# Performance work log

Hardware: AMD Instinct MI355X
Metric: run time of the kernel (lower is better)

Reference implementation:

```python
import jax, jax.numpy as jnp
import numpy as np

B, H, W = 64, 512, 512
HW = H * W
MIN_, MAX_ = 100, 100          # seeds sampled per image (bg, fg)
MIN_P, MAX_P = 0.3, 0.3        # candidate-pool fractions
FG_ERODE_K, FG_ERODE_ITER = 11, 1
KSZ = 3                        # dilation kernel for seed maps
IGNORE_IDX = -255
N_BG = int(MIN_P * H * W)      # static bottom-n pool size
EPS = 1e-8


def _minpool2d(x, k):  # morphological erosion of binary map (geodesic border)
    return jax.lax.reduce_window(x, np.inf, jax.lax.min, (k, k), (1, 1), 'SAME')


def _maxpool3d(x, k):  # morphological dilation over (b,h,w)
    return jax.lax.reduce_window(x, -np.inf, jax.lax.max, (1, k, k), (1, 1, 1), 'SAME')


def _gumbel(u):
    return -jnp.log(-jnp.log(u))


def _one_sample(cam, u_fg, u_bg, th):
    # cam: [H,W] in [0,1]; u_fg/u_bg: [HW] uniform(0,1); th: scalar threshold
    cam_q = jnp.floor(cam * 255.0)
    th = jnp.where(th == 0.0, 1.0, jnp.where(th == 255.0, 254.0, th))
    deg = cam.min() == cam.max()  # degenerate map -> no seeds
    roi = (cam_q > th).astype(jnp.float32)
    for _ in range(FG_ERODE_ITER):
        roi = _minpool2d(roi, FG_ERODE_K)

    # ---- foreground: top-n of cam*roi, weighted sample max_ w/o replacement
    camr = (cam * roi + EPS).reshape(HW)
    n_fg = jnp.floor(MAX_P * roi.sum()).astype(jnp.int32)
    order = jnp.argsort(-camr, stable=True)                 # descending stable
    rank = jnp.zeros(HW, jnp.int32).at[order].set(jnp.arange(HW, dtype=jnp.int32))
    mask = rank < n_fg
    logp = jnp.log(jnp.where(mask, camr, 1.0))              # weighted: p = cam value
    score = jnp.where(mask, logp + _gumbel(u_fg), -jnp.inf) # Gumbel top-k == multinomial w/o repl.
    _, sel = jax.lax.top_k(score, MAX_)
    valid = (jnp.arange(MAX_) < jnp.minimum(MAX_, n_fg)) & (n_fg > 0) & (~deg)
    fg = jnp.zeros(HW, jnp.int32).at[sel].set(valid.astype(jnp.int32))

    # ---- background: bottom-n of cam, weighted by relu(1-cam)+eps
    camb = (cam + EPS).reshape(HW)
    orderb = jnp.argsort(camb, stable=True)                 # ascending stable
    rankb = jnp.zeros(HW, jnp.int32).at[orderb].set(jnp.arange(HW, dtype=jnp.int32))
    maskb = rankb < N_BG
    pb = jax.nn.relu(1.0 - camb) + EPS
    scoreb = jnp.where(maskb, jnp.log(pb) + _gumbel(u_bg), -jnp.inf)
    _, selb = jax.lax.top_k(scoreb, MIN_)
    validb = (jnp.arange(MIN_) < min(MIN_, N_BG)) & (~deg)
    bg = jnp.zeros(HW, jnp.int32).at[selb].set(validb.astype(jnp.int32))

    return fg.reshape(H, W), bg.reshape(H, W)


def setup_inputs() -> dict:
    key = jax.random.key(0)
    k1, k2, k3, k4 = jax.random.split(key, 4)
    x = jax.random.uniform(k1, (B, 1, H, W), dtype=jnp.float32)
    roi_thresh = jax.random.randint(k2, (B,), 0, 200).astype(jnp.float32)
    u_fg = jax.random.uniform(k3, (B, HW), dtype=jnp.float32, minval=1e-6, maxval=1.0)
    u_bg = jax.random.uniform(k4, (B, HW), dtype=jnp.float32, minval=1e-6, maxval=1.0)
    return {"x": x, "roi_thresh": roi_thresh, "u_fg": u_fg, "u_bg": u_bg}


def reference(x, roi_thresh, u_fg, u_bg):
    cam = x[:, 0]  # [B,H,W]
    all_fg, all_bg = jax.vmap(_one_sample)(cam, u_fg, u_bg, roi_thresh)
    if KSZ > 1:
        all_fg = (_maxpool3d(all_fg.astype(jnp.float32), KSZ) > 0.5).astype(jnp.int32)
        all_bg = (_maxpool3d(all_bg.astype(jnp.float32), KSZ) > 0.5).astype(jnp.int32)
    outer = all_fg + all_bg
    all_fg = jnp.where(outer == 2, 0, all_fg)
    all_bg = jnp.where(outer == 2, 0, all_bg)
    out = jnp.full((B, H, W), IGNORE_IDX, dtype=jnp.int32)
    out = jnp.where(all_fg == 1, 1, out)
    out = jnp.where(all_bg == 1, 0, out)
    return out
```

## Files before the change

kernel.cpp:

```cpp
#include <hip/hip_runtime.h>

typedef unsigned int u32;

#define BB 64
#define HH 512
#define WW 512
#define HWP 262144
#define WPI 8192
#define NBV 8192
#define NBS 4096
#define EPSF 1e-8f
#define NBGK 78643
#define CAND_CAP 4096
#define SEL_CAP 128
#define PN 20


__device__ __forceinline__ int vbucket(float vb){
    int b = (int)(vb * 8192.0f);
    b = b < 0 ? 0 : b;
    return b > (NBV-1) ? (NBV-1) : b;
}
__device__ __forceinline__ int sbucket(float s){
    float a = (s + 24.0f) * (4096.0f / 44.0f);
    a = fmaxf(a, 0.0f);
    int b = (int)a;
    return b > (NBS-1) ? (NBS-1) : b;
}
__device__ __forceinline__ u32 flipf(float s){
    u32 u = __float_as_uint(s);
    u32 m = (u & 0x80000000u) ? 0xFFFFFFFFu : 0x80000000u;
    return u ^ m;
}


__global__ __launch_bounds__(256) void k_prep(const float* __restrict__ x,
        const float* __restrict__ thr, u32* __restrict__ roi0,
        u32* __restrict__ ghist_bg, u32* __restrict__ minb, u32* __restrict__ maxb,
        int* __restrict__ out)
{
    __shared__ u32 hist[NBV];
    __shared__ u32 words[256];
    for (int i = threadIdx.x; i < NBV; i += 256) hist[i] = 0u;
    words[threadIdx.x] = 0u;
    __syncthreads();
    int img = blockIdx.x >> 5;
    int blk = blockIdx.x & 31;
    int t = threadIdx.x;
    size_t base4 = (size_t)img * (HWP/4) + (size_t)blk * 2048;
    const float4* c4 = (const float4*)x + base4;
    int4* o4 = (int4*)out + base4;
    float th = thr[img];
    th = (th == 0.0f) ? 1.0f : ((th == 255.0f) ? 254.0f : th);
    u32 mn = 0xFFFFFFFFu, mx = 0u;
    #pragma unroll
    for (int k = 0; k < 8; k++){
        float4 v4 = c4[k*256 + t];
        float vv[4] = {v4.x, v4.y, v4.z, v4.w};
        u32 nib = 0u;
        #pragma unroll
        for (int c = 0; c < 4; c++){
            float v = vv[c];
            u32 ub = __float_as_uint(v);
            mn = mn < ub ? mn : ub;
            mx = mx > ub ? mx : ub;
            if (floorf(v * 255.0f) > th) nib |= (1u << c);
            atomicAdd(&hist[vbucket(v + EPSF)], 1u);
        }
        if (nib) atomicOr(&words[k*32 + (t>>3)], nib << ((t&7)*4));
        o4[k*256 + t] = make_int4(-255,-255,-255,-255);
    }
    for (int o = 32; o >= 1; o >>= 1){
        u32 m2 = __shfl_down(mn, o); mn = mn < m2 ? mn : m2;
        u32 m3 = __shfl_down(mx, o); mx = mx > m3 ? mx : m3;
    }
    if ((t & 63) == 0){
        atomicMin(&minb[img], mn);
        atomicMax(&maxb[img], mx);
    }
    __syncthreads();
    roi0[(size_t)img * WPI + blk*256 + t] = words[t];
    for (int i = t; i < NBV; i += 256){
        u32 h = hist[i];
        if (h) atomicAdd(&ghist_bg[(size_t)img*NBV + i], h);
    }
}

__global__ __launch_bounds__(256) void k_erode(const u32* __restrict__ roi0,
        u32* __restrict__ roiE, u32* __restrict__ roiSum)
{
    __shared__ u32 A[WPI];
    __shared__ u32 Bm[WPI];
    int img = blockIdx.x, t = threadIdx.x;
    const u32* src = roi0 + (size_t)img * WPI;
    for (int i = t; i < WPI; i += 256) A[i] = src[i];
    __syncthreads();
    for (int i = t; i < WPI; i += 256){
        int wr = i & 15;
        u32 cur = A[i];
        u32 left  = (wr > 0)  ? A[i-1] : 0xFFFFFFFFu;
        u32 right = (wr < 15) ? A[i+1] : 0xFFFFFFFFu;
        u32 res = cur;
        #pragma unroll
        for (int d = 1; d <= 5; d++){
            res &= (cur >> d) | (right << (32 - d));
            res &= (cur << d) | (left  >> (32 - d));
        }
        Bm[i] = res;
    }
    __syncthreads();
    if (t == 0) A[0] = 0u;
    __syncthreads();
    u32 cnt = 0u;
    u32* dst = roiE + (size_t)img * WPI;
    for (int i = t; i < WPI; i += 256){
        int r = i >> 4;
        u32 res = 0xFFFFFFFFu;
        #pragma unroll
        for (int d = -5; d <= 5; d++){
            int rr = r + d;
            if (rr >= 0 && rr < HH) res &= Bm[i + d*16];
        }
        dst[i] = res;
        cnt += __popc(res);
    }
    for (int o = 32; o >= 1; o >>= 1) cnt += __shfl_down(cnt, o);
    if ((t & 63) == 0) atomicAdd(&A[0], cnt);
    __syncthreads();
    if (t == 0) roiSum[img] = A[0];
}

__global__ __launch_bounds__(256) void k_fghist(const float* __restrict__ x, const u32* __restrict__ roiE,
        u32* __restrict__ ghist_fg)
{
    __shared__ u32 hist[NBV];
    __shared__ u32 words[256];
    for (int i = threadIdx.x; i < NBV; i += 256) hist[i] = 0u;
    int img = blockIdx.x >> 5;
    int blk = blockIdx.x & 31;
    int t = threadIdx.x;
    words[t] = roiE[(size_t)img*WPI + blk*256 + t];
    __syncthreads();
    const float4* c4 = (const float4*)x + (size_t)img * (HWP/4) + (size_t)blk * 2048;
    #pragma unroll
    for (int k = 0; k < 8; k++){
        u32 nib = (words[k*32 + (t>>3)] >> ((t&7)*4)) & 0xFu;
        if (nib){
            float4 v4 = c4[k*256 + t];
            float vv[4] = {v4.x, v4.y, v4.z, v4.w};
            #pragma unroll
            for (int c = 0; c < 4; c++){
                if ((nib >> c) & 1u) atomicAdd(&hist[vbucket(vv[c] + EPSF)], 1u);
            }
        }
    }
    __syncthreads();
    for (int i = t; i < NBV; i += 256){
        u32 h = hist[i];
        if (h) atomicAdd(&ghist_fg[(size_t)img*NBV + i], h);
    }
}

__global__ __launch_bounds__(256) void k_bound1(const u32* __restrict__ ghf, const u32* __restrict__ ghb,
        const u32* __restrict__ minb, const u32* __restrict__ maxb, const u32* __restrict__ roiSum,
        int* __restrict__ prm)
{
    int b = blockIdx.x, t = threadIdx.x;
    __shared__ int partial[256];
    __shared__ int res[2];
    int deg = (minb[b] == maxb[b]) ? 1 : 0;
    int nfg = (int)floorf(0.3f * (float)(int)roiSum[b]);
    int Bf = -1, rf = 0, Bb = -1, rb = 0;
    if (!deg && nfg > 0){
        const u32* hh = ghf + (size_t)b * NBV;
        int s = 0;
        for (int i = 0; i < 32; i++) s += (int)hh[NBV-1 - (t*32+i)];
        partial[t] = s;
        __syncthreads();
        if (t == 0){
            int cum = 0, q = 0;
            for (; q < 256; q++){ if (cum + partial[q] >= nfg) break; cum += partial[q]; }
            for (int i = 0; i < 32; i++){
                int bkt = NBV-1 - (q*32+i);
                int h = (int)hh[bkt];
                if (cum + h >= nfg){ res[0] = bkt; res[1] = nfg - cum; break; }
                cum += h;
            }
        }
        __syncthreads();
        Bf = res[0]; rf = res[1];
        __syncthreads();
    }
    if (!deg){
        const u32* hh = ghb + (size_t)b * NBV;
        int s = 0;
        for (int i = 0; i < 32; i++) s += (int)hh[t*32+i];
        partial[t] = s;
        __syncthreads();
        if (t == 0){
            int cum = 0, q = 0;
            for (; q < 256; q++){ if (cum + partial[q] >= NBGK) break; cum += partial[q]; }
            for (int i = 0; i < 32; i++){
                int bkt = q*32+i;
                int h = (int)hh[bkt];
                if (cum + h >= NBGK){ res[0] = bkt; res[1] = NBGK - cum; break; }
                cum += h;
            }
        }
        __syncthreads();
        Bb = res[0]; rb = res[1];
    }
    if (t == 0){
        int* p = prm + b * PN;
        p[0] = nfg; p[1] = deg; p[2] = Bf; p[3] = rf; p[4] = Bb; p[5] = rb;
    }
}

__global__ __launch_bounds__(256) void k_collect1(const float* __restrict__ x, const u32* __restrict__ roiE,
        const int* __restrict__ prm,
        uint2* __restrict__ candF, u32* __restrict__ cntF,
        uint2* __restrict__ candB, u32* __restrict__ cntB)
{
    __shared__ u32 words[256];
    int img = blockIdx.x >> 5;
    int blk = blockIdx.x & 31;
    int t = threadIdx.x;
    int Bf = prm[img*PN + 2];
    int Bb = prm[img*PN + 4];
    words[t] = roiE[(size_t)img*WPI + blk*256 + t];
    __syncthreads();
    const float4* c4 = (const float4*)x + (size_t)img * (HWP/4) + (size_t)blk * 2048;
    #pragma unroll
    for (int k = 0; k < 8; k++){
        float4 v4 = c4[k*256 + t];
        float vv[4] = {v4.x, v4.y, v4.z, v4.w};
        u32 nib = (words[k*32 + (t>>3)] >> ((t&7)*4)) & 0xFu;
        int pix0 = blk*8192 + k*1024 + t*4;
        #pragma unroll
        for (int c = 0; c < 4; c++){
            float vb = vv[c] + EPSF;
            int bkt = vbucket(vb);
            int pix = pix0 + c;
            if (bkt == Bb){
                u32 q = atomicAdd(&cntB[img], 1u);
                if (q < CAND_CAP) candB[(size_t)img*CAND_CAP + q] = make_uint2(__float_as_uint(vb), (u32)pix);
            }
            if (bkt == Bf && ((nib >> c) & 1u)){
                u32 q = atomicAdd(&cntF[img], 1u);
                if (q < CAND_CAP) candF[(size_t)img*CAND_CAP + q] = make_uint2(__float_as_uint(vb), (u32)pix);
            }
        }
    }
}

__global__ __launch_bounds__(256) void k_resolve1(const uint2* __restrict__ candF, const u32* __restrict__ cntF,
        const uint2* __restrict__ candB, const u32* __restrict__ cntB, int* __restrict__ prm)
{
    int b = blockIdx.x, t = threadIdx.x;
    __shared__ uint2 c[CAND_CAP];
    int rf = prm[b*PN + 3];
    if (rf > 0){
        int m = (int)cntF[b]; m = m < CAND_CAP ? m : CAND_CAP;
        for (int i = t; i < m; i += 256) c[i] = candF[(size_t)b*CAND_CAP + i];
        __syncthreads();
        for (int i = t; i < m; i += 256){
            u32 ki = c[i].x, xi = c[i].y;
            int r = 0;
            for (int j = 0; j < m; j++){
                u32 kj = c[j].x, xj = c[j].y;
                r += (kj > ki) || (kj == ki && xj < xi);
            }
            if (r == rf - 1){ prm[b*PN + 6] = (int)ki; prm[b*PN + 7] = (int)xi; }
        }
    } else if (t == 0){
        prm[b*PN + 6] = (int)0xFFFFFFFFu; prm[b*PN + 7] = -1;
    }
    __syncthreads();
    int rb = prm[b*PN + 5];
    if (rb > 0){
        int m = (int)cntB[b]; m = m < CAND_CAP ? m : CAND_CAP;
        for (int i = t; i < m; i += 256) c[i] = candB[(size_t)b*CAND_CAP + i];
        __syncthreads();
        for (int i = t; i < m; i += 256){
            u32 ki = c[i].x, xi = c[i].y;
            int r = 0;
            for (int j = 0; j < m; j++){
                u32 kj = c[j].x, xj = c[j].y;
                r += (kj < ki) || (kj == ki && xj < xi);
            }
            if (r == rb - 1){ prm[b*PN + 8] = (int)ki; prm[b*PN + 9] = (int)xi; }
        }
    } else if (t == 0){
        prm[b*PN + 8] = 0; prm[b*PN + 9] = -1;
    }
}

__global__ __launch_bounds__(256) void k_shist(const float* __restrict__ x, const u32* __restrict__ roiE,
        const float* __restrict__ ufg, const float* __restrict__ ubg, const int* __restrict__ prm,
        u32* __restrict__ shfG, u32* __restrict__ shbG)
{
    __shared__ u32 hf[NBS];
    __shared__ u32 hb[NBS];
    __shared__ u32 words[256];
    for (int i = threadIdx.x; i < NBS; i += 256){ hf[i] = 0u; hb[i] = 0u; }
    int img = blockIdx.x >> 5;
    int blk = blockIdx.x & 31;
    int t = threadIdx.x;
    words[t] = roiE[(size_t)img*WPI + blk*256 + t];
    __syncthreads();
    const int* p = prm + img*PN;
    u32 ubf = (u32)p[6]; int ibf = p[7];
    u32 ubb = (u32)p[8]; int ibb = p[9];
    size_t b4 = (size_t)img * (HWP/4) + (size_t)blk * 2048;
    const float4* c4 = (const float4*)x + b4;
    const float4* uf4 = (const float4*)ufg + b4;
    const float4* ub4 = (const float4*)ubg + b4;
    #pragma unroll
    for (int k = 0; k < 8; k++){
        float4 v4 = c4[k*256 + t];
        float vv[4] = {v4.x, v4.y, v4.z, v4.w};
        u32 nib = (words[k*32 + (t>>3)] >> ((t&7)*4)) & 0xFu;
        int pix0 = blk*8192 + k*1024 + t*4;
        float vbv[4]; bool fm[4], bm[4]; bool anyf = false, anyb = false;
        #pragma unroll
        for (int c = 0; c < 4; c++){
            float vb = vv[c] + EPSF;
            vbv[c] = vb;
            u32 bu = __float_as_uint(vb);
            int pix = pix0 + c;
            fm[c] = ((nib >> c) & 1u) && (bu > ubf || (bu == ubf && pix <= ibf));
            bm[c] = (bu < ubb || (bu == ubb && pix <= ibb));
            anyf |= fm[c]; anyb |= bm[c];
        }
        if (anyf){
            float4 u4 = uf4[k*256 + t];
            float uu[4] = {u4.x, u4.y, u4.z, u4.w};
            #pragma unroll
            for (int c = 0; c < 4; c++){
                if (fm[c]){
                    float s = logf(vbv[c]) - logf(-logf(uu[c]));
                    atomicAdd(&hf[sbucket(s)], 1u);
                }
            }
        }
        if (anyb){
            float4 u4 = ub4[k*256 + t];
            float uu[4] = {u4.x, u4.y, u4.z, u4.w};
            #pragma unroll
            for (int c = 0; c < 4; c++){
                if (bm[c]){
                    float pb = fmaxf(1.0f - vbv[c], 0.0f) + EPSF;
                    float s = logf(pb) - logf(-logf(uu[c]));
                    atomicAdd(&hb[sbucket(s)], 1u);
                }
            }
        }
    }
    __syncthreads();
    for (int i = t; i < NBS; i += 256){
        u32 h = hf[i]; if (h) atomicAdd(&shfG[(size_t)img*NBS + i], h);
        h = hb[i];     if (h) atomicAdd(&shbG[(size_t)img*NBS + i], h);
    }
}

__global__ __launch_bounds__(256) void k_bound2(const u32* __restrict__ shfG, const u32* __restrict__ shbG,
        int* __restrict__ prm)
{
    int b = blockIdx.x, t = threadIdx.x;
    __shared__ int partial[256];
    __shared__ int res[2];
    int* p = prm + b*PN;
    int nfg = p[0], deg = p[1];
    int kf = (deg || nfg <= 0) ? 0 : (nfg < 100 ? nfg : 100);
    int kb = deg ? 0 : 100;
    int sbf = 0x7FFFFFFF, needf = 0, sbb = 0x7FFFFFFF, needb = 0;
    if (kf > 0){
        const u32* hh = shfG + (size_t)b * NBS;
        int s = 0;
        for (int i = 0; i < 16; i++) s += (int)hh[NBS-1 - (t*16+i)];
        partial[t] = s;
        __syncthreads();
        if (t == 0){
            int cum = 0, q = 0;
            for (; q < 256; q++){ if (cum + partial[q] >= kf) break; cum += partial[q]; }
            for (int i = 0; i < 16; i++){
                int bkt = NBS-1 - (q*16+i);
                int h = (int)hh[bkt];
                if (cum + h >= kf){ res[0] = bkt; res[1] = kf - cum; break; }
                cum += h;
            }
        }
        __syncthreads();
        sbf = res[0]; needf = res[1];
        __syncthreads();
    }
    if (kb > 0){
        const u32* hh = shbG + (size_t)b * NBS;
        int s = 0;
        for (int i = 0; i < 16; i++) s += (int)hh[NBS-1 - (t*16+i)];
        partial[t] = s;
        __syncthreads();
        if (t == 0){
            int cum = 0, q = 0;
            for (; q < 256; q++){ if (cum + partial[q] >= kb) break; cum += partial[q]; }
            for (int i = 0; i < 16; i++){
                int bkt = NBS-1 - (q*16+i);
                int h = (int)hh[bkt];
                if (cum + h >= kb){ res[0] = bkt; res[1] = kb - cum; break; }
                cum += h;
            }
        }
        __syncthreads();
        sbb = res[0]; needb = res[1];
    }
    if (t == 0){
        p[10] = sbf; p[12] = needf; p[13] = sbb; p[15] = needb; p[16] = kf; p[17] = kb;
    }
}

__global__ __launch_bounds__(256) void k_collect2(const float* __restrict__ x, const u32* __restrict__ roiE,
        const float* __restrict__ ufg, const float* __restrict__ ubg, const int* __restrict__ prm,
        uint2* __restrict__ selF, u32* __restrict__ cntSelF, uint2* __restrict__ scandF, u32* __restrict__ cntScF,
        uint2* __restrict__ selB, u32* __restrict__ cntSelB, uint2* __restrict__ scandB, u32* __restrict__ cntScB)
{
    __shared__ u32 words[256];
    int img = blockIdx.x >> 5;
    int blk = blockIdx.x & 31;
    int t = threadIdx.x;
    words[t] = roiE[(size_t)img*WPI + blk*256 + t];
    __syncthreads();
    const int* p = prm + img*PN;
    u32 ubf = (u32)p[6]; int ibf = p[7];
    u32 ubb = (u32)p[8]; int ibb = p[9];
    int sbf = p[10], sbb = p[13];
    size_t b4 = (size_t)img * (HWP/4) + (size_t)blk * 2048;
    const float4* c4 = (const float4*)x + b4;
    const float4* uf4 = (const float4*)ufg + b4;
    const float4* ub4 = (const float4*)ubg + b4;
    #pragma unroll
    for (int k = 0; k < 8; k++){
        float4 v4 = c4[k*256 + t];
        float vv[4] = {v4.x, v4.y, v4.z, v4.w};
        u32 nib = (words[k*32 + (t>>3)] >> ((t&7)*4)) & 0xFu;
        int pix0 = blk*8192 + k*1024 + t*4;
        float vbv[4]; bool fm[4], bm[4]; bool anyf = false, anyb = false;
        #pragma unroll
        for (int c = 0; c < 4; c++){
            float vb = vv[c] + EPSF;
            vbv[c] = vb;
            u32 bu = __float_as_uint(vb);
            int pix = pix0 + c;
            fm[c] = ((nib >> c) & 1u) && (bu > ubf || (bu == ubf && pix <= ibf));
            bm[c] = (bu < ubb || (bu == ubb && pix <= ibb));
            anyf |= fm[c]; anyb |= bm[c];
        }
        if (anyf){
            float4 u4 = uf4[k*256 + t];
            float uu[4] = {u4.x, u4.y, u4.z, u4.w};
            #pragma unroll
            for (int c = 0; c < 4; c++){
                if (fm[c]){
                    float s = logf(vbv[c]) - logf(-logf(uu[c]));
                    int sb = sbucket(s);
                    if (sb > sbf){
                        u32 q = atomicAdd(&cntSelF[img], 1u);
                        if (q < SEL_CAP) selF[(size_t)img*SEL_CAP + q] = make_uint2(flipf(s), (u32)(pix0 + c));
                    } else if (sb == sbf){
                        u32 q = atomicAdd(&cntScF[img], 1u);
                        if (q < CAND_CAP) scandF[(size_t)img*CAND_CAP + q] = make_uint2(flipf(s), (u32)(pix0 + c));
                    }
                }
            }
        }
        if (anyb){
            float4 u4 = ub4[k*256 + t];
            float uu[4] = {u4.x, u4.y, u4.z, u4.w};
            #pragma unroll
            for (int c = 0; c < 4; c++){
                if (bm[c]){
                    float pb = fmaxf(1.0f - vbv[c], 0.0f) + EPSF;
                    float s = logf(pb) - logf(-logf(uu[c]));
                    int sb = sbucket(s);
                    if (sb > sbb){
                        u32 q = atomicAdd(&cntSelB[img], 1u);
                        if (q < SEL_CAP) selB[(size_t)img*SEL_CAP + q] = make_uint2(flipf(s), (u32)(pix0 + c));
                    } else if (sb == sbb){
                        u32 q = atomicAdd(&cntScB[img], 1u);
                        if (q < CAND_CAP) scandB[(size_t)img*CAND_CAP + q] = make_uint2(flipf(s), (u32)(pix0 + c));
                    }
                }
            }
        }
    }
}

__global__ __launch_bounds__(256) void k_final(
        const uint2* __restrict__ selF, const u32* __restrict__ cntSelF,
        const uint2* __restrict__ scandF, const u32* __restrict__ cntScF,
        const uint2* __restrict__ selB, const u32* __restrict__ cntSelB,
        const uint2* __restrict__ scandB, const u32* __restrict__ cntScB,
        const int* __restrict__ prm, int* __restrict__ out)
{
    int b = blockIdx.x, t = threadIdx.x;
    __shared__ uint2 c[CAND_CAP];
    __shared__ int seedF[SEL_CAP];
    __shared__ int seedB[SEL_CAP];
    __shared__ int nF, nB;
    const int* p = prm + b*PN;
    int needf = p[12], needb = p[15];

    int c0 = (int)cntSelF[b]; c0 = c0 < SEL_CAP ? c0 : SEL_CAP;
    for (int i = t; i < c0; i += 256) seedF[i] = (int)selF[(size_t)b*SEL_CAP + i].y;
    int m = (int)cntScF[b]; m = m < CAND_CAP ? m : CAND_CAP;
    for (int i = t; i < m; i += 256) c[i] = scandF[(size_t)b*CAND_CAP + i];
    if (t == 0){ nF = c0; nB = 0; }
    __syncthreads();
    for (int i = t; i < m; i += 256){
        u32 ki = c[i].x, xi = c[i].y;
        int r = 0;
        for (int j = 0; j < m; j++){
            u32 kj = c[j].x, xj = c[j].y;
            r += (kj > ki) || (kj == ki && xj < xi);
        }
        if (r < needf){
            int q = atomicAdd(&nF, 1);
            if (q < SEL_CAP) seedF[q] = (int)xi;
        }
    }
    __syncthreads();
    int fN = nF; fN = fN < SEL_CAP ? fN : SEL_CAP;
    __syncthreads();

    int c0b = (int)cntSelB[b]; c0b = c0b < SEL_CAP ? c0b : SEL_CAP;
    for (int i = t; i < c0b; i += 256) seedB[i] = (int)selB[(size_t)b*SEL_CAP + i].y;
    int mb = (int)cntScB[b]; mb = mb < CAND_CAP ? mb : CAND_CAP;
    for (int i = t; i < mb; i += 256) c[i] = scandB[(size_t)b*CAND_CAP + i];
    if (t == 0) nB = c0b;
    __syncthreads();
    for (int i = t; i < mb; i += 256){
        u32 ki = c[i].x, xi = c[i].y;
        int r = 0;
        for (int j = 0; j < mb; j++){
            u32 kj = c[j].x, xj = c[j].y;
            r += (kj > ki) || (kj == ki && xj < xi);
        }
        if (r < needb){
            int q = atomicAdd(&nB, 1);
            if (q < SEL_CAP) seedB[q] = (int)xi;
        }
    }
    __syncthreads();
    int bN = nB; bN = bN < SEL_CAP ? bN : SEL_CAP;
    __syncthreads();

    int* outp = out + (size_t)b * HWP;
    for (int task = t; task < fN * 9; task += 256){
        int s = seedF[task / 9];
        int o = task % 9;
        int y = (s >> 9) + (o / 3) - 1;
        int xx = (s & 511) + (o % 3) - 1;
        if (y < 0 || y >= HH || xx < 0 || xx >= WW) continue;
        bool conf = false;
        for (int j = 0; j < bN; j++){
            int sb2 = seedB[j];
            int dy = y - (sb2 >> 9); if (dy < 0) dy = -dy;
            int dx = xx - (sb2 & 511); if (dx < 0) dx = -dx;
            if (dy <= 1 && dx <= 1){ conf = true; break; }
        }
        if (!conf) outp[y * WW + xx] = 1;
    }
    for (int task = t; task < bN * 9; task += 256){
        int s = seedB[task / 9];
        int o = task % 9;
        int y = (s >> 9) + (o / 3) - 1;
        int xx = (s & 511) + (o % 3) - 1;
        if (y < 0 || y >= HH || xx < 0 || xx >= WW) continue;
        bool conf = false;
        for (int j = 0; j < fN; j++){
            int sf2 = seedF[j];
            int dy = y - (sf2 >> 9); if (dy < 0) dy = -dy;
            int dx = xx - (sf2 & 511); if (dx < 0) dx = -dx;
            if (dy <= 1 && dx <= 1){ conf = true; break; }
        }
        if (!conf) outp[y * WW + xx] = 0;
    }
}

extern "C" void kernel_launch(void* const* d_in, const int* in_sizes, int n_in,
                              void* d_out, int out_size, void* d_ws, size_t ws_size,
                              hipStream_t stream)
{
    (void)in_sizes; (void)n_in; (void)out_size; (void)ws_size;
    const float* x   = (const float*)d_in[0];
    const float* thr = (const float*)d_in[1];
    const float* ufg = (const float*)d_in[2];
    const float* ubg = (const float*)d_in[3];
    int* out = (int*)d_out;
    char* ws = (char*)d_ws;

    size_t off = 0;
    auto carve = [&](size_t bytes) -> char* {
        char* ptr = ws + off;
        off = (off + bytes + 255) & ~(size_t)255;
        return ptr;
    };
    u32* ghist_bg = (u32*)carve((size_t)BB*NBV*4);
    u32* ghist_fg = (u32*)carve((size_t)BB*NBV*4);
    u32* shf      = (u32*)carve((size_t)BB*NBS*4);
    u32* shb      = (u32*)carve((size_t)BB*NBS*4);
    u32* cnts     = (u32*)carve((size_t)6*BB*4);
    u32* maxb     = (u32*)carve((size_t)BB*4);
    u32* roiSum   = (u32*)carve((size_t)BB*4);
    size_t zero_bytes = off;
    u32* minb     = (u32*)carve((size_t)BB*4);
    size_t minb_off = (size_t)((char*)minb - ws);
    u32* roi0     = (u32*)carve((size_t)BB*WPI*4);
    u32* roiE     = (u32*)carve((size_t)BB*WPI*4);
    int* prm      = (int*)carve((size_t)BB*PN*4);
    uint2* candF  = (uint2*)carve((size_t)BB*CAND_CAP*8);
    uint2* candB  = (uint2*)carve((size_t)BB*CAND_CAP*8);
    uint2* scandF = (uint2*)carve((size_t)BB*CAND_CAP*8);
    uint2* scandB = (uint2*)carve((size_t)BB*CAND_CAP*8);
    uint2* selF   = (uint2*)carve((size_t)BB*SEL_CAP*8);
    uint2* selB   = (uint2*)carve((size_t)BB*SEL_CAP*8);
    u32* cntF = cnts, *cntB = cnts + BB, *cntSelF = cnts + 2*BB,
       *cntScF = cnts + 3*BB, *cntSelB = cnts + 4*BB, *cntScB = cnts + 5*BB;

    hipMemsetAsync(ws, 0, zero_bytes, stream);
    hipMemsetAsync(ws + minb_off, 0xFF, (size_t)BB*4, stream);

    k_prep    <<<2048, 256, 0, stream>>>(x, thr, roi0, ghist_bg, minb, maxb, out);
    k_erode   <<<64,   256, 0, stream>>>(roi0, roiE, roiSum);
    k_fghist  <<<2048, 256, 0, stream>>>(x, roiE, ghist_fg);
    k_bound1  <<<64,   256, 0, stream>>>(ghist_fg, ghist_bg, minb, maxb, roiSum, prm);
    k_collect1<<<2048, 256, 0, stream>>>(x, roiE, prm, candF, cntF, candB, cntB);
    k_resolve1<<<64,   256, 0, stream>>>(candF, cntF, candB, cntB, prm);
    k_shist   <<<2048, 256, 0, stream>>>(x, roiE, ufg, ubg, prm, shf, shb);
    k_bound2  <<<64,   256, 0, stream>>>(shf, shb, prm);
    k_collect2<<<2048, 256, 0, stream>>>(x, roiE, ufg, ubg, prm,
                                         selF, cntSelF, scandF, cntScF,
                                         selB, cntSelB, scandB, cntScB);
    k_final   <<<64,   256, 0, stream>>>(selF, cntSelF, scandF, cntScF,
                                         selB, cntSelB, scandB, cntScB, prm, out);
}
```

Measured before the change: 495.9 us.

## Fuse per-image ROI, histograms, bounds and candidate resolve into one block kernel

Six kernels (prep, erode, fg histogram, bound, collect, resolve) are merged into one 1024-thread block per image that keeps the ROI bitmap, both histograms and the candidate lists in shared memory, with no global atomics or intermediate buffers. The output fill and seed painting move into a new 2048-block paint kernel that handles 16-row stripes, and the later kernels use an interleaved image/block mapping. This removes launches and global round trips, but phase one now runs on only 64 blocks, each streaming a whole 1 MB image three times, so it may be limited by low parallelism.

New measurement: 470.3 us. 1.05x faster.

```diff
diff --git a/kernel.cpp b/kernel.cpp
--- a/kernel.cpp
+++ b/kernel.cpp
@@ -14,6 +14,7 @@
 #define CAND_CAP 4096
 #define SEL_CAP 128
 #define PN 20
+#define TA 1024
 
 
 __device__ __forceinline__ int vbucket(float vb){
@@ -33,29 +34,30 @@
     return u ^ m;
 }
 
-
-__global__ __launch_bounds__(256) void k_prep(const float* __restrict__ x,
-        const float* __restrict__ thr, u32* __restrict__ roi0,
-        u32* __restrict__ ghist_bg, u32* __restrict__ minb, u32* __restrict__ maxb,
-        int* __restrict__ out)
-{
-    __shared__ u32 hist[NBV];
-    __shared__ u32 words[256];
-    for (int i = threadIdx.x; i < NBV; i += 256) hist[i] = 0u;
-    words[threadIdx.x] = 0u;
-    __syncthreads();
-    int img = blockIdx.x >> 5;
-    int blk = blockIdx.x & 31;
-    int t = threadIdx.x;
-    size_t base4 = (size_t)img * (HWP/4) + (size_t)blk * 2048;
-    const float4* c4 = (const float4*)x + base4;
-    int4* o4 = (int4*)out + base4;
+__global__ __launch_bounds__(TA) void k_roi(const float* __restrict__ x,
+        const float* __restrict__ thr, u32* __restrict__ roiE, int* __restrict__ prm)
+{
+    __shared__ __align__(16) u32 S[3*WPI];
+    __shared__ int partial[TA];
+    __shared__ int res2[2];
+    __shared__ u32 sMin, sMax, sCnt;
+    __shared__ int cF, cB;
+    u32* A  = S;
+    u32* HB = S + WPI;
+    u32* HF = S + 2*WPI;
+    int img = blockIdx.x, t = threadIdx.x;
+
+    for (int i = t; i < WPI; i += TA){ A[i] = 0u; HB[i] = 0u; }
+    if (t == 0){ sMin = 0xFFFFFFFFu; sMax = 0u; sCnt = 0u; }
+    __syncthreads();
+
+    const float4* c4 = (const float4*)x + (size_t)img * (HWP/4);
     float th = thr[img];
     th = (th == 0.0f) ? 1.0f : ((th == 255.0f) ? 254.0f : th);
     u32 mn = 0xFFFFFFFFu, mx = 0u;
-    #pragma unroll
-    for (int k = 0; k < 8; k++){
-        float4 v4 = c4[k*256 + t];
+    for (int k = 0; k < 64; k++){
+        int fi = k*TA + t;
+        float4 v4 = c4[fi];
         float vv[4] = {v4.x, v4.y, v4.z, v4.w};
         u32 nib = 0u;
         #pragma unroll
@@ -65,37 +67,18 @@
             mn = mn < ub ? mn : ub;
             mx = mx > ub ? mx : ub;
             if (floorf(v * 255.0f) > th) nib |= (1u << c);
-            atomicAdd(&hist[vbucket(v + EPSF)], 1u);
-        }
-        if (nib) atomicOr(&words[k*32 + (t>>3)], nib << ((t&7)*4));
-        o4[k*256 + t] = make_int4(-255,-255,-255,-255);
+            atomicAdd(&HB[vbucket(v + EPSF)], 1u);
+        }
+        if (nib) atomicOr(&A[fi >> 3], nib << ((fi & 7) * 4));
     }
     for (int o = 32; o >= 1; o >>= 1){
         u32 m2 = __shfl_down(mn, o); mn = mn < m2 ? mn : m2;
         u32 m3 = __shfl_down(mx, o); mx = mx > m3 ? mx : m3;
     }
-    if ((t & 63) == 0){
-        atomicMin(&minb[img], mn);
-        atomicMax(&maxb[img], mx);
-    }
-    __syncthreads();
-    roi0[(size_t)img * WPI + blk*256 + t] = words[t];
-    for (int i = t; i < NBV; i += 256){
-        u32 h = hist[i];
-        if (h) atomicAdd(&ghist_bg[(size_t)img*NBV + i], h);
-    }
-}
-
-__global__ __launch_bounds__(256) void k_erode(const u32* __restrict__ roi0,
-        u32* __restrict__ roiE, u32* __restrict__ roiSum)
-{
-    __shared__ u32 A[WPI];
-    __shared__ u32 Bm[WPI];
-    int img = blockIdx.x, t = threadIdx.x;
-    const u32* src = roi0 + (size_t)img * WPI;
-    for (int i = t; i < WPI; i += 256) A[i] = src[i];
-    __syncthreads();
-    for (int i = t; i < WPI; i += 256){
+    if ((t & 63) == 0){ atomicMin(&sMin, mn); atomicMax(&sMax, mx); }
+    __syncthreads();
+
+    for (int i = t; i < WPI; i += TA){
         int wr = i & 15;
         u32 cur = A[i];
         u32 left  = (wr > 0)  ? A[i-1] : 0xFFFFFFFFu;
@@ -106,193 +89,151 @@
             res &= (cur >> d) | (right << (32 - d));
             res &= (cur << d) | (left  >> (32 - d));
         }
-        Bm[i] = res;
-    }
-    __syncthreads();
-    if (t == 0) A[0] = 0u;
+        HF[i] = res;
+    }
     __syncthreads();
     u32 cnt = 0u;
     u32* dst = roiE + (size_t)img * WPI;
-    for (int i = t; i < WPI; i += 256){
+    for (int i = t; i < WPI; i += TA){
         int r = i >> 4;
         u32 res = 0xFFFFFFFFu;
         #pragma unroll
         for (int d = -5; d <= 5; d++){
             int rr = r + d;
-            if (rr >= 0 && rr < HH) res &= Bm[i + d*16];
-        }
+            if (rr >= 0 && rr < HH) res &= HF[i + d*16];
+        }
+        A[i] = res;
         dst[i] = res;
         cnt += __popc(res);
     }
     for (int o = 32; o >= 1; o >>= 1) cnt += __shfl_down(cnt, o);
-    if ((t & 63) == 0) atomicAdd(&A[0], cnt);
-    __syncthreads();
-    if (t == 0) roiSum[img] = A[0];
-}
-
-__global__ __launch_bounds__(256) void k_fghist(const float* __restrict__ x, const u32* __restrict__ roiE,
-        u32* __restrict__ ghist_fg)
-{
-    __shared__ u32 hist[NBV];
-    __shared__ u32 words[256];
-    for (int i = threadIdx.x; i < NBV; i += 256) hist[i] = 0u;
-    int img = blockIdx.x >> 5;
-    int blk = blockIdx.x & 31;
-    int t = threadIdx.x;
-    words[t] = roiE[(size_t)img*WPI + blk*256 + t];
-    __syncthreads();
-    const float4* c4 = (const float4*)x + (size_t)img * (HWP/4) + (size_t)blk * 2048;
-    #pragma unroll
-    for (int k = 0; k < 8; k++){
-        u32 nib = (words[k*32 + (t>>3)] >> ((t&7)*4)) & 0xFu;
+    if ((t & 63) == 0) atomicAdd(&sCnt, cnt);
+    __syncthreads();
+
+    int roiSum = (int)sCnt;
+    int deg = (sMin == sMax) ? 1 : 0;
+    int nfg = (int)floorf(0.3f * (float)roiSum);
+
+    for (int i = t; i < WPI; i += TA) HF[i] = 0u;
+    __syncthreads();
+    for (int k = 0; k < 64; k++){
+        int fi = k*TA + t;
+        u32 nib = (A[fi >> 3] >> ((fi & 7) * 4)) & 0xFu;
         if (nib){
-            float4 v4 = c4[k*256 + t];
+            float4 v4 = c4[fi];
             float vv[4] = {v4.x, v4.y, v4.z, v4.w};
             #pragma unroll
             for (int c = 0; c < 4; c++){
-                if ((nib >> c) & 1u) atomicAdd(&hist[vbucket(vv[c] + EPSF)], 1u);
-            }
-        }
-    }
-    __syncthreads();
-    for (int i = t; i < NBV; i += 256){
-        u32 h = hist[i];
-        if (h) atomicAdd(&ghist_fg[(size_t)img*NBV + i], h);
-    }
-}
-
-__global__ __launch_bounds__(256) void k_bound1(const u32* __restrict__ ghf, const u32* __restrict__ ghb,
-        const u32* __restrict__ minb, const u32* __restrict__ maxb, const u32* __restrict__ roiSum,
-        int* __restrict__ prm)
-{
-    int b = blockIdx.x, t = threadIdx.x;
-    __shared__ int partial[256];
-    __shared__ int res[2];
-    int deg = (minb[b] == maxb[b]) ? 1 : 0;
-    int nfg = (int)floorf(0.3f * (float)(int)roiSum[b]);
+                if ((nib >> c) & 1u) atomicAdd(&HF[vbucket(vv[c] + EPSF)], 1u);
+            }
+        }
+    }
+    __syncthreads();
+
     int Bf = -1, rf = 0, Bb = -1, rb = 0;
     if (!deg && nfg > 0){
-        const u32* hh = ghf + (size_t)b * NBV;
         int s = 0;
-        for (int i = 0; i < 32; i++) s += (int)hh[NBV-1 - (t*32+i)];
+        for (int i = 0; i < 8; i++) s += (int)HF[NBV-1 - (t*8+i)];
         partial[t] = s;
         __syncthreads();
         if (t == 0){
             int cum = 0, q = 0;
-            for (; q < 256; q++){ if (cum + partial[q] >= nfg) break; cum += partial[q]; }
-            for (int i = 0; i < 32; i++){
-                int bkt = NBV-1 - (q*32+i);
-                int h = (int)hh[bkt];
-                if (cum + h >= nfg){ res[0] = bkt; res[1] = nfg - cum; break; }
+            for (; q < TA; q++){ if (cum + partial[q] >= nfg) break; cum += partial[q]; }
+            for (int i = 0; i < 8; i++){
+                int bkt = NBV-1 - (q*8+i);
+                int h = (int)HF[bkt];
+                if (cum + h >= nfg){ res2[0] = bkt; res2[1] = nfg - cum; break; }
                 cum += h;
             }
         }
         __syncthreads();
-        Bf = res[0]; rf = res[1];
+        Bf = res2[0]; rf = res2[1];
         __syncthreads();
     }
     if (!deg){
-        const u32* hh = ghb + (size_t)b * NBV;
         int s = 0;
-        for (int i = 0; i < 32; i++) s += (int)hh[t*32+i];
+        for (int i = 0; i < 8; i++) s += (int)HB[t*8+i];
         partial[t] = s;
         __syncthreads();
         if (t == 0){
             int cum = 0, q = 0;
-            for (; q < 256; q++){ if (cum + partial[q] >= NBGK) break; cum += partial[q]; }
-            for (int i = 0; i < 32; i++){
-                int bkt = q*32+i;
-                int h = (int)hh[bkt];
-                if (cum + h >= NBGK){ res[0] = bkt; res[1] = NBGK - cum; break; }
+            for (; q < TA; q++){ if (cum + partial[q] >= NBGK) break; cum += partial[q]; }
+            for (int i = 0; i < 8; i++){
+                int bkt = q*8+i;
+                int h = (int)HB[bkt];
+                if (cum + h >= NBGK){ res2[0] = bkt; res2[1] = NBGK - cum; break; }
                 cum += h;
             }
         }
         __syncthreads();
-        Bb = res[0]; rb = res[1];
-    }
-    if (t == 0){
-        int* p = prm + b * PN;
-        p[0] = nfg; p[1] = deg; p[2] = Bf; p[3] = rf; p[4] = Bb; p[5] = rb;
-    }
-}
-
-__global__ __launch_bounds__(256) void k_collect1(const float* __restrict__ x, const u32* __restrict__ roiE,
-        const int* __restrict__ prm,
-        uint2* __restrict__ candF, u32* __restrict__ cntF,
-        uint2* __restrict__ candB, u32* __restrict__ cntB)
-{
-    __shared__ u32 words[256];
-    int img = blockIdx.x >> 5;
-    int blk = blockIdx.x & 31;
-    int t = threadIdx.x;
-    int Bf = prm[img*PN + 2];
-    int Bb = prm[img*PN + 4];
-    words[t] = roiE[(size_t)img*WPI + blk*256 + t];
-    __syncthreads();
-    const float4* c4 = (const float4*)x + (size_t)img * (HWP/4) + (size_t)blk * 2048;
-    #pragma unroll
-    for (int k = 0; k < 8; k++){
-        float4 v4 = c4[k*256 + t];
+        Bb = res2[0]; rb = res2[1];
+        __syncthreads();
+    }
+
+    uint2* candF = (uint2*)HB;
+    uint2* candB = (uint2*)HF;
+    if (t == 0){ cF = 0; cB = 0; }
+    __syncthreads();
+    for (int k = 0; k < 64; k++){
+        int fi = k*TA + t;
+        float4 v4 = c4[fi];
         float vv[4] = {v4.x, v4.y, v4.z, v4.w};
-        u32 nib = (words[k*32 + (t>>3)] >> ((t&7)*4)) & 0xFu;
-        int pix0 = blk*8192 + k*1024 + t*4;
+        u32 nib = (A[fi >> 3] >> ((fi & 7) * 4)) & 0xFu;
         #pragma unroll
         for (int c = 0; c < 4; c++){
             float vb = vv[c] + EPSF;
             int bkt = vbucket(vb);
-            int pix = pix0 + c;
+            int pix = fi*4 + c;
             if (bkt == Bb){
-                u32 q = atomicAdd(&cntB[img], 1u);
-                if (q < CAND_CAP) candB[(size_t)img*CAND_CAP + q] = make_uint2(__float_as_uint(vb), (u32)pix);
+                int q = atomicAdd(&cB, 1);
+                if (q < CAND_CAP) candB[q] = make_uint2(__float_as_uint(vb), (u32)pix);
             }
             if (bkt == Bf && ((nib >> c) & 1u)){
-                u32 q = atomicAdd(&cntF[img], 1u);
-                if (q < CAND_CAP) candF[(size_t)img*CAND_CAP + q] = make_uint2(__float_as_uint(vb), (u32)pix);
-            }
-        }
-    }
-}
-
-__global__ __launch_bounds__(256) void k_resolve1(const uint2* __restrict__ candF, const u32* __restrict__ cntF,
-        const uint2* __restrict__ candB, const u32* __restrict__ cntB, int* __restrict__ prm)
-{
-    int b = blockIdx.x, t = threadIdx.x;
-    __shared__ uint2 c[CAND_CAP];
-    int rf = prm[b*PN + 3];
+                int q = atomicAdd(&cF, 1);
+                if (q < CAND_CAP) candF[q] = make_uint2(__float_as_uint(vb), (u32)pix);
+            }
+        }
+    }
+    __syncthreads();
+
+    int* p = prm + img * PN;
     if (rf > 0){
-        int m = (int)cntF[b]; m = m < CAND_CAP ? m : CAND_CAP;
-        for (int i = t; i < m; i += 256) c[i] = candF[(size_t)b*CAND_CAP + i];
-        __syncthreads();
-        for (int i = t; i < m; i += 256){
-            u32 ki = c[i].x, xi = c[i].y;
+        int m = cF; m = m < CAND_CAP ? m : CAND_CAP;
+        for (int i = t; i < m; i += TA){
+            u32 ki = candF[i].x, xi = candF[i].y;
             int r = 0;
             for (int j = 0; j < m; j++){
-                u32 kj = c[j].x, xj = c[j].y;
+                u32 kj = candF[j].x, xj = candF[j].y;
                 r += (kj > ki) || (kj == ki && xj < xi);
             }
-            if (r == rf - 1){ prm[b*PN + 6] = (int)ki; prm[b*PN + 7] = (int)xi; }
+            if (r == rf - 1){ p[6] = (int)ki; p[7] = (int)xi; }
         }
     } else if (t == 0){
-        prm[b*PN + 6] = (int)0xFFFFFFFFu; prm[b*PN + 7] = -1;
-    }
-    __syncthreads();
-    int rb = prm[b*PN + 5];
+        p[6] = (int)0xFFFFFFFFu; p[7] = -1;
+    }
     if (rb > 0){
-        int m = (int)cntB[b]; m = m < CAND_CAP ? m : CAND_CAP;
-        for (int i = t; i < m; i += 256) c[i] = candB[(size_t)b*CAND_CAP + i];
-        __syncthreads();
-        for (int i = t; i < m; i += 256){
-            u32 ki = c[i].x, xi = c[i].y;
+        int m = cB; m = m < CAND_CAP ? m : CAND_CAP;
+        for (int i = t; i < m; i += TA){
+            u32 ki = candB[i].x, xi = candB[i].y;
             int r = 0;
             for (int j = 0; j < m; j++){
-                u32 kj = c[j].x, xj = c[j].y;
+                u32 kj = candB[j].x, xj = candB[j].y;
                 r += (kj < ki) || (kj == ki && xj < xi);
             }
-            if (r == rb - 1){ prm[b*PN + 8] = (int)ki; prm[b*PN + 9] = (int)xi; }
+            if (r == rb - 1){ p[8] = (int)ki; p[9] = (int)xi; }
         }
     } else if (t == 0){
-        prm[b*PN + 8] = 0; prm[b*PN + 9] = -1;
-    }
+        p[8] = 0; p[9] = -1;
+    }
+    if (t == 0){
+        p[0] = nfg; p[1] = deg; p[2] = Bf; p[3] = rf; p[4] = Bb; p[5] = rb;
+    }
+}
+
+__device__ __forceinline__ void imgblk(int bid, int& img, int& blk){
+    int r = bid & 7, s = bid >> 3;
+    img = ((s >> 5) << 3) | r;
+    blk = s & 31;
 }
 
 __global__ __launch_bounds__(256) void k_shist(const float* __restrict__ x, const u32* __restrict__ roiE,
@@ -303,8 +244,8 @@
     __shared__ u32 hb[NBS];
     __shared__ u32 words[256];
     for (int i = threadIdx.x; i < NBS; i += 256){ hf[i] = 0u; hb[i] = 0u; }
-    int img = blockIdx.x >> 5;
-    int blk = blockIdx.x & 31;
+    int img, blk;
+    imgblk(blockIdx.x, img, blk);
     int t = threadIdx.x;
     words[t] = roiE[(size_t)img*WPI + blk*256 + t];
     __syncthreads();
@@ -424,8 +365,8 @@
         uint2* __restrict__ selB, u32* __restrict__ cntSelB, uint2* __restrict__ scandB, u32* __restrict__ cntScB)
 {
     __shared__ u32 words[256];
-    int img = blockIdx.x >> 5;
-    int blk = blockIdx.x & 31;
+    int img, blk;
+    imgblk(blockIdx.x, img, blk);
     int t = threadIdx.x;
     words[t] = roiE[(size_t)img*WPI + blk*256 + t];
     __syncthreads();
@@ -494,12 +435,14 @@
     }
 }
 
-__global__ __launch_bounds__(256) void k_final(
+__global__ __launch_bounds__(256) void k_seeds(
         const uint2* __restrict__ selF, const u32* __restrict__ cntSelF,
         const uint2* __restrict__ scandF, const u32* __restrict__ cntScF,
         const uint2* __restrict__ selB, const u32* __restrict__ cntSelB,
         const uint2* __restrict__ scandB, const u32* __restrict__ cntScB,
-        const int* __restrict__ prm, int* __restrict__ out)
+        const int* __restrict__ prm,
+        int* __restrict__ gSeedF, int* __restrict__ gnF,
+        int* __restrict__ gSeedB, int* __restrict__ gnB)
 {
     int b = blockIdx.x, t = threadIdx.x;
     __shared__ uint2 c[CAND_CAP];
@@ -551,18 +494,37 @@
     }
     __syncthreads();
     int bN = nB; bN = bN < SEL_CAP ? bN : SEL_CAP;
-    __syncthreads();
-
-    int* outp = out + (size_t)b * HWP;
+
+    for (int i = t; i < fN; i += 256) gSeedF[b*SEL_CAP + i] = seedF[i];
+    for (int i = t; i < bN; i += 256) gSeedB[b*SEL_CAP + i] = seedB[i];
+    if (t == 0){ gnF[b] = fN; gnB[b] = bN; }
+}
+
+__global__ __launch_bounds__(256) void k_paint(
+        const int* __restrict__ gSeedF, const int* __restrict__ gnF,
+        const int* __restrict__ gSeedB, const int* __restrict__ gnB,
+        int* __restrict__ out)
+{
+    __shared__ int sF[SEL_CAP], sB[SEL_CAP];
+    int img = blockIdx.x >> 5, blk = blockIdx.x & 31, t = threadIdx.x;
+    int fN = gnF[img]; fN = fN < SEL_CAP ? fN : SEL_CAP;
+    int bN = gnB[img]; bN = bN < SEL_CAP ? bN : SEL_CAP;
+    for (int i = t; i < fN; i += 256) sF[i] = gSeedF[img*SEL_CAP + i];
+    for (int i = t; i < bN; i += 256) sB[i] = gSeedB[img*SEL_CAP + i];
+    int4* o4 = (int4*)(out + (size_t)img*HWP + blk*8192);
+    for (int i = t; i < 2048; i += 256) o4[i] = make_int4(-255,-255,-255,-255);
+    __syncthreads();
+    int row0 = blk * 16;
+    int* outp = out + (size_t)img*HWP;
     for (int task = t; task < fN * 9; task += 256){
-        int s = seedF[task / 9];
+        int s = sF[task / 9];
         int o = task % 9;
         int y = (s >> 9) + (o / 3) - 1;
         int xx = (s & 511) + (o % 3) - 1;
-        if (y < 0 || y >= HH || xx < 0 || xx >= WW) continue;
+        if (y < row0 || y >= row0 + 16 || xx < 0 || xx >= WW) continue;
         bool conf = false;
         for (int j = 0; j < bN; j++){
-            int sb2 = seedB[j];
+            int sb2 = sB[j];
             int dy = y - (sb2 >> 9); if (dy < 0) dy = -dy;
             int dx = xx - (sb2 & 511); if (dx < 0) dx = -dx;
             if (dy <= 1 && dx <= 1){ conf = true; break; }
@@ -570,14 +532,14 @@
         if (!conf) outp[y * WW + xx] = 1;
     }
     for (int task = t; task < bN * 9; task += 256){
-        int s = seedB[task / 9];
+        int s = sB[task / 9];
         int o = task % 9;
         int y = (s >> 9) + (o / 3) - 1;
         int xx = (s & 511) + (o % 3) - 1;
-        if (y < 0 || y >= HH || xx < 0 || xx >= WW) continue;
+        if (y < row0 || y >= row0 + 16 || xx < 0 || xx >= WW) continue;
         bool conf = false;
         for (int j = 0; j < fN; j++){
-            int sf2 = seedF[j];
+            int sf2 = sF[j];
             int dy = y - (sf2 >> 9); if (dy < 0) dy = -dy;
             int dx = xx - (sf2 & 511); if (dx < 0) dx = -dx;
             if (dy <= 1 && dx <= 1){ conf = true; break; }
@@ -604,42 +566,32 @@
         off = (off + bytes + 255) & ~(size_t)255;
         return ptr;
     };
-    u32* ghist_bg = (u32*)carve((size_t)BB*NBV*4);
-    u32* ghist_fg = (u32*)carve((size_t)BB*NBV*4);
     u32* shf      = (u32*)carve((size_t)BB*NBS*4);
     u32* shb      = (u32*)carve((size_t)BB*NBS*4);
-    u32* cnts     = (u32*)carve((size_t)6*BB*4);
-    u32* maxb     = (u32*)carve((size_t)BB*4);
-    u32* roiSum   = (u32*)carve((size_t)BB*4);
+    u32* cnts     = (u32*)carve((size_t)4*BB*4);
     size_t zero_bytes = off;
-    u32* minb     = (u32*)carve((size_t)BB*4);
-    size_t minb_off = (size_t)((char*)minb - ws);
-    u32* roi0     = (u32*)carve((size_t)BB*WPI*4);
     u32* roiE     = (u32*)carve((size_t)BB*WPI*4);
     int* prm      = (int*)carve((size_t)BB*PN*4);
-    uint2* candF  = (uint2*)carve((size_t)BB*CAND_CAP*8);
-    uint2* candB  = (uint2*)carve((size_t)BB*CAND_CAP*8);
     uint2* scandF = (uint2*)carve((size_t)BB*CAND_CAP*8);
     uint2* scandB = (uint2*)carve((size_t)BB*CAND_CAP*8);
     uint2* selF   = (uint2*)carve((size_t)BB*SEL_CAP*8);
     uint2* selB   = (uint2*)carve((size_t)BB*SEL_CAP*8);
-    u32* cntF = cnts, *cntB = cnts + BB, *cntSelF = cnts + 2*BB,
-       *cntScF = cnts + 3*BB, *cntSelB = cnts + 4*BB, *cntScB = cnts + 5*BB;
+    int* gSeedF   = (int*)carve((size_t)BB*SEL_CAP*4);
+    int* gSeedB   = (int*)carve((size_t)BB*SEL_CAP*4);
+    int* gnF      = (int*)carve((size_t)BB*4);
+    int* gnB      = (int*)carve((size_t)BB*4);
+    u32* cntSelF = cnts, *cntScF = cnts + BB, *cntSelB = cnts + 2*BB, *cntScB = cnts + 3*BB;
 
     hipMemsetAsync(ws, 0, zero_bytes, stream);
-    hipMemsetAsync(ws + minb_off, 0xFF, (size_t)BB*4, stream);
-
-    k_prep    <<<2048, 256, 0, stream>>>(x, thr, roi0, ghist_bg, minb, maxb, out);
-    k_erode   <<<64,   256, 0, stream>>>(roi0, roiE, roiSum);
-    k_fghist  <<<2048, 256, 0, stream>>>(x, roiE, ghist_fg);
-    k_bound1  <<<64,   256, 0, stream>>>(ghist_fg, ghist_bg, minb, maxb, roiSum, prm);
-    k_collect1<<<2048, 256, 0, stream>>>(x, roiE, prm, candF, cntF, candB, cntB);
-    k_resolve1<<<64,   256, 0, stream>>>(candF, cntF, candB, cntB, prm);
+
+    k_roi     <<<64,   TA,  0, stream>>>(x, thr, roiE, prm);
     k_shist   <<<2048, 256, 0, stream>>>(x, roiE, ufg, ubg, prm, shf, shb);
     k_bound2  <<<64,   256, 0, stream>>>(shf, shb, prm);
     k_collect2<<<2048, 256, 0, stream>>>(x, roiE, ufg, ubg, prm,
                                          selF, cntSelF, scandF, cntScF,
                                          selB, cntSelB, scandB, cntScB);
-    k_final   <<<64,   256, 0, stream>>>(selF, cntSelF, scandF, cntScF,
-                                         selB, cntSelB, scandB, cntScB, prm, out);
-}
+    k_seeds   <<<64,   256, 0, stream>>>(selF, cntSelF, scandF, cntScF,
+                                         selB, cntSelB, scandB, cntScB, prm,
+                                         gSeedF, gnF, gSeedB, gnB);
+    k_paint   <<<2048, 256, 0, stream>>>(gSeedF, gnF, gSeedB, gnB, out);
+}
```
